# Performance work log

Measured on AMD Instinct MI355X. Metric: run time of the kernel, lower is better.

## Reference

```python
import jax, jax.numpy as jnp
import numpy as np
from jax.scipy.linalg import expm

LATENT, HID, OMEGA, TRANZ, K = 64, 40, 9, 3, 262144


def _linear_params(key, out_d, in_d):
    # equinox Linear default init: U(-1/sqrt(in), 1/sqrt(in)) for weight and bias
    lim = 1.0 / np.sqrt(in_d)
    kw, kb = jax.random.split(key)
    W = jax.random.uniform(kw, (out_d, in_d), minval=-lim, maxval=lim, dtype=jnp.float32)
    b = jax.random.uniform(kb, (out_d,), minval=-lim, maxval=lim, dtype=jnp.float32)
    return W, b


def setup_inputs() -> dict:
    key = jax.random.key(0)
    keys = jax.random.split(key, 7)
    W_o1, b_o1 = _linear_params(keys[0], HID, LATENT)
    W_o2, b_o2 = _linear_params(keys[1], HID, HID)
    W_o3, b_o3 = _linear_params(keys[2], OMEGA, HID)
    W_t1, b_t1 = _linear_params(keys[3], HID, LATENT)
    W_t2, b_t2 = _linear_params(keys[4], HID, HID)
    W_t3, b_t3 = _linear_params(keys[5], TRANZ, HID)
    x = jax.random.normal(keys[6], (LATENT, K), dtype=jnp.float32)
    return {
        "x": x,
        "W_o1": W_o1, "b_o1": b_o1, "W_o2": W_o2, "b_o2": b_o2, "W_o3": W_o3, "b_o3": b_o3,
        "W_t1": W_t1, "b_t1": b_t1, "W_t2": W_t2, "b_t2": b_t2, "W_t3": W_t3, "b_t3": b_t3,
    }


def _exp_omega(omega_flat):
    # omega_flat: (9, K); expm of each column reshaped to 3x3, flattened -> (K, 9)
    f = lambda col: expm(col.reshape(3, 3)).reshape(9)
    return jax.vmap(f, in_axes=1)(omega_flat)


def reference(x, W_o1, b_o1, W_o2, b_o2, W_o3, b_o3,
              W_t1, b_t1, W_t2, b_t2, W_t3, b_t3):
    relu = jax.nn.relu
    # omega branch (note: original applies relu after EVERY layer, incl. last)
    h = relu(W_o1 @ x + b_o1[:, None])
    h = relu(W_o2 @ h + b_o2[:, None])
    omega = relu(W_o3 @ h + b_o3[:, None])          # (9, K)
    rotation = _exp_omega(omega).T                   # (9, K)
    # translation branch
    t = relu(W_t1 @ x + b_t1[:, None])
    t = relu(W_t2 @ t + b_t2[:, None])
    translation = relu(W_t3 @ t + b_t3[:, None])     # (3, K)
    return (omega, rotation, translation)
```

## Files before the change

### kernel.cpp

```cpp
#include <hip/hip_runtime.h>
#include <hip/hip_bf16.h>

#define KC 262144

typedef __attribute__((ext_vector_type(8))) short bf16x8;
typedef __attribute__((ext_vector_type(4))) float f32x4;
typedef unsigned short u16;
typedef unsigned int u32;

__device__ __forceinline__ u16 f2bf(float f) {
    u32 u = __float_as_uint(f);
    return (u16)((u + 0x7fffu + ((u >> 16) & 1u)) >> 16);
}
__device__ __forceinline__ u32 pk2(float a, float b) {
    u16 lo = __bfloat16_as_ushort(__float2bfloat16(a));
    u16 hi = __bfloat16_as_ushort(__float2bfloat16(b));
    return (u32)lo | ((u32)hi << 16);
}
__device__ __forceinline__ float bf2f(u32 h) {
    return __uint_as_float(h << 16);
}

__global__ __launch_bounds__(256) void prep(
    const float* __restrict__ Wo1, const float* __restrict__ bo1,
    const float* __restrict__ Wo2, const float* __restrict__ bo2,
    const float* __restrict__ Wo3, const float* __restrict__ bo3,
    const float* __restrict__ Wt1, const float* __restrict__ bt1,
    const float* __restrict__ Wt2, const float* __restrict__ bt2,
    const float* __restrict__ Wt3, const float* __restrict__ bt3,
    u16* __restrict__ ws)
{
    u16* W1s = ws;
    u16* W2s = ws + 5120;
    u16* W3s = ws + 12800;
    float* b1s = (float*)(ws + 14336);
    const int t0 = blockIdx.x * 256 + threadIdx.x;
    const int NT = gridDim.x * 256;

    for (int i = t0; i < 5120; i += NT) {
        int r = i >> 6, k = i & 63;
        float v = (r < 40) ? Wo1[r * 64 + k] : Wt1[(r - 40) * 64 + k];
        W1s[i] = f2bf(v);
    }
    for (int i = t0; i < 7680; i += NT) {
        int r = i / 96, k = i - r * 96;
        float v = 0.f;
        if (r < 40) {
            if (k < 40) v = Wo2[r * 40 + k];
            else if (k == 80) v = bo2[r];
        } else {
            int rr = r - 40;
            if (k >= 40 && k < 80) v = Wt2[rr * 40 + (k - 40)];
            else if (k == 80) v = bt2[rr];
        }
        W2s[i] = f2bf(v);
    }
    for (int i = t0; i < 1536; i += NT) {
        int r = i / 96, k = i - r * 96;
        float v = 0.f;
        if (r < 9) {
            if (k < 40) v = Wo3[r * 40 + k];
            else if (k == 80) v = bo3[r];
        } else if (r < 12) {
            int rr = r - 9;
            if (k >= 40 && k < 80) v = Wt3[rr * 40 + (k - 40)];
            else if (k == 80) v = bt3[rr];
        }
        W3s[i] = f2bf(v);
    }
    for (int i = t0; i < 80; i += NT)
        b1s[i] = (i < 40) ? bo1[i] : bt1[i - 40];
}

__global__ __launch_bounds__(256, 2) void mlp_mfma(
    const float* __restrict__ x, const u16* __restrict__ ws,
    float* __restrict__ out)
{
    const u16* W1s = ws;
    const u16* W2s = ws + 5120;
    const u16* W3s = ws + 12800;
    const float* b1s = (const float*)(ws + 14336);

    __shared__ float slab[4][64 * 36];

    const int tid = threadIdx.x;
    const int wid = tid >> 6;
    const int lane = tid & 63;
    const int g = lane >> 4;
    const int c = lane & 15;
    const int wgid = blockIdx.x * 4 + wid;
    const int cbase = wgid * 64;

    float* xstage = &slab[wid][0];
    u16* hstp = (u16*)&slab[wid][0];

    bf16x8 A1[5][2], A3[3];
    f32x4 b1v[5];
#pragma unroll
    for (int m = 0; m < 5; ++m) {
#pragma unroll
        for (int s = 0; s < 2; ++s)
            A1[m][s] = *(const bf16x8*)(W1s + (16 * m + c) * 64 + 32 * s + 8 * g);
        b1v[m] = *(const f32x4*)(b1s + 16 * m + 4 * g);
    }
    bf16x8 A2[5][3];
#pragma unroll
    for (int m = 0; m < 5; ++m)
#pragma unroll
        for (int s = 0; s < 3; ++s)
            if (!(s == 0 && m >= 3))
                A2[m][s] = *(const bf16x8*)(W2s + (16 * m + c) * 96 + 32 * s + 8 * g);
#pragma unroll
    for (int s = 0; s < 3; ++s)
        A3[s] = *(const bf16x8*)(W3s + c * 96 + 32 * s + 8 * g);

    const char* gbase = (const char*)x
        + ((size_t)(lane >> 3) * KC + (size_t)(cbase + 4 * (lane & 7))) * 4;
    const int wb = (lane >> 3) * 36 + 4 * (lane & 7);

    u32 w0[4], w1[4];

#pragma unroll
    for (int ch = 0; ch < 2; ++ch) {
        float4 G[8];
#pragma unroll
        for (int i = 0; i < 8; ++i)
            G[i] = *(const float4*)(gbase + (size_t)i * 8 * KC * 4 + ch * 128);
#pragma unroll
        for (int i = 0; i < 8; ++i)
            *(float4*)&xstage[wb + i * 288] = G[i];

        bf16x8 xv[2][2];
#pragma unroll
        for (int tl = 0; tl < 2; ++tl)
#pragma unroll
            for (int s = 0; s < 2; ++s) {
                union { u32 u[4]; bf16x8 v; } uu;
#pragma unroll
                for (int p = 0; p < 4; ++p) {
                    float lo = xstage[(8 * g + 32 * s + 2 * p) * 36 + 16 * tl + c];
                    float hi = xstage[(8 * g + 32 * s + 2 * p + 1) * 36 + 16 * tl + c];
                    uu.u[p] = pk2(lo, hi);
                }
                xv[tl][s] = uu.v;
            }

        {
            uint2 z;
            z.x = (g == 0) ? 0x00003f80u : 0u;
            z.y = 0u;
            *(uint2*)&hstp[c * 120 + 80 + 4 * g] = z;
        }

#pragma unroll
        for (int tl = 0; tl < 2; ++tl) {
            const int gt = 2 * ch + tl;

            f32x4 a1[5];
#pragma unroll
            for (int m = 0; m < 5; ++m) a1[m] = b1v[m];
#pragma unroll
            for (int s = 0; s < 2; ++s)
#pragma unroll
                for (int m = 0; m < 5; ++m)
                    a1[m] = __builtin_amdgcn_mfma_f32_16x16x32_bf16(
                        A1[m][s], xv[tl][s], a1[m], 0, 0, 0);
#pragma unroll
            for (int m = 0; m < 5; ++m) {
                uint2 w;
                w.x = pk2(fmaxf(a1[m][0], 0.f), fmaxf(a1[m][1], 0.f));
                w.y = pk2(fmaxf(a1[m][2], 0.f), fmaxf(a1[m][3], 0.f));
                *(uint2*)&hstp[c * 120 + 16 * m + 4 * g] = w;
            }

            f32x4 a2[5];
#pragma unroll
            for (int m = 0; m < 5; ++m) a2[m] = f32x4{0.f, 0.f, 0.f, 0.f};
#pragma unroll
            for (int s = 0; s < 3; ++s) {
                bf16x8 hb = *(const bf16x8*)&hstp[c * 120 + 32 * s + 8 * g];
#pragma unroll
                for (int m = 0; m < 5; ++m)
                    if (!(s == 0 && m >= 3))
                        a2[m] = __builtin_amdgcn_mfma_f32_16x16x32_bf16(
                            A2[m][s], hb, a2[m], 0, 0, 0);
            }
#pragma unroll
            for (int m = 0; m < 5; ++m) {
                uint2 w;
                w.x = pk2(fmaxf(a2[m][0], 0.f), fmaxf(a2[m][1], 0.f));
                w.y = pk2(fmaxf(a2[m][2], 0.f), fmaxf(a2[m][3], 0.f));
                *(uint2*)&hstp[c * 120 + 16 * m + 4 * g] = w;
            }

            f32x4 a3 = f32x4{0.f, 0.f, 0.f, 0.f};
#pragma unroll
            for (int s = 0; s < 3; ++s) {
                bf16x8 hb = *(const bf16x8*)&hstp[c * 120 + 32 * s + 8 * g];
                a3 = __builtin_amdgcn_mfma_f32_16x16x32_bf16(
                    A3[s], hb, a3, 0, 0, 0);
            }
            w0[gt] = pk2(fmaxf(a3[0], 0.f), fmaxf(a3[1], 0.f));
            w1[gt] = pk2(fmaxf(a3[2], 0.f), fmaxf(a3[3], 0.f));
        }
    }

    {
        const int T = lane >> 4;
        const int cp = lane & 15;
        const int s0 = cp, s1 = 16 + cp, s2 = 32 + cp;

        auto selT = [&](u32 v0, u32 v1, u32 v2, u32 v3) -> u32 {
            u32 lo = (T & 1) ? v1 : v0;
            u32 hi = (T & 1) ? v3 : v2;
            return (T & 2) ? hi : lo;
        };
        u32 q0 = selT((u32)__shfl((int)w0[0], s0), (u32)__shfl((int)w0[1], s0),
                      (u32)__shfl((int)w0[2], s0), (u32)__shfl((int)w0[3], s0));
        u32 q1 = selT((u32)__shfl((int)w1[0], s0), (u32)__shfl((int)w1[1], s0),
                      (u32)__shfl((int)w1[2], s0), (u32)__shfl((int)w1[3], s0));
        u32 q2 = selT((u32)__shfl((int)w0[0], s1), (u32)__shfl((int)w0[1], s1),
                      (u32)__shfl((int)w0[2], s1), (u32)__shfl((int)w0[3], s1));
        u32 q3 = selT((u32)__shfl((int)w1[0], s1), (u32)__shfl((int)w1[1], s1),
                      (u32)__shfl((int)w1[2], s1), (u32)__shfl((int)w1[3], s1));
        u32 q4 = selT((u32)__shfl((int)w0[0], s2), (u32)__shfl((int)w0[1], s2),
                      (u32)__shfl((int)w0[2], s2), (u32)__shfl((int)w0[3], s2));
        u32 q5 = selT((u32)__shfl((int)w1[0], s2), (u32)__shfl((int)w1[1], s2),
                      (u32)__shfl((int)w1[2], s2), (u32)__shfl((int)w1[3], s2));

        float om[9];
        om[0] = bf2f(q0 & 0xffffu); om[1] = bf2f(q0 >> 16);
        om[2] = bf2f(q1 & 0xffffu); om[3] = bf2f(q1 >> 16);
        om[4] = bf2f(q2 & 0xffffu); om[5] = bf2f(q2 >> 16);
        om[6] = bf2f(q3 & 0xffffu); om[7] = bf2f(q3 >> 16);
        om[8] = bf2f(q4 & 0xffffu);
        float tr0 = bf2f(q4 >> 16);
        float tr1 = bf2f(q5 & 0xffffu);
        float tr2 = bf2f(q5 >> 16);

        const size_t ob = (size_t)cbase + lane;
#pragma unroll
        for (int j = 0; j < 9; ++j)
            out[(size_t)j * KC + ob] = om[j];
        out[(size_t)18 * KC + ob] = tr0;
        out[(size_t)19 * KC + ob] = tr1;
        out[(size_t)20 * KC + ob] = tr2;

        float B[9];
#pragma unroll
        for (int i = 0; i < 9; ++i) B[i] = om[i] * (1.0f / 32.0f);
        float T9[9] = {1.f, 0.f, 0.f, 0.f, 1.f, 0.f, 0.f, 0.f, 1.f};
#pragma unroll
        for (int m = 9; m >= 1; --m) {
            float U[9];
#pragma unroll
            for (int rr = 0; rr < 3; ++rr)
#pragma unroll
                for (int cc = 0; cc < 3; ++cc)
                    U[rr * 3 + cc] = B[rr * 3 + 0] * T9[0 * 3 + cc]
                                   + B[rr * 3 + 1] * T9[1 * 3 + cc]
                                   + B[rr * 3 + 2] * T9[2 * 3 + cc];
            const float s = 1.0f / (float)m;
#pragma unroll
            for (int i = 0; i < 9; ++i)
                T9[i] = U[i] * s + ((i == 0 || i == 4 || i == 8) ? 1.0f : 0.0f);
        }
#pragma unroll
        for (int q = 0; q < 5; ++q) {
            float U[9];
#pragma unroll
            for (int rr = 0; rr < 3; ++rr)
#pragma unroll
                for (int cc = 0; cc < 3; ++cc)
                    U[rr * 3 + cc] = T9[rr * 3 + 0] * T9[0 * 3 + cc]
                                   + T9[rr * 3 + 1] * T9[1 * 3 + cc]
                                   + T9[rr * 3 + 2] * T9[2 * 3 + cc];
#pragma unroll
            for (int i = 0; i < 9; ++i) T9[i] = U[i];
        }
#pragma unroll
        for (int j = 0; j < 9; ++j)
            out[(size_t)(9 + j) * KC + ob] = T9[j];
    }
}

extern "C" void kernel_launch(void* const* d_in, const int* in_sizes, int n_in,
                              void* d_out, int out_size, void* d_ws, size_t ws_size,
                              hipStream_t stream) {
    const float* x   = (const float*)d_in[0];
    const float* Wo1 = (const float*)d_in[1];
    const float* bo1 = (const float*)d_in[2];
    const float* Wo2 = (const float*)d_in[3];
    const float* bo2 = (const float*)d_in[4];
    const float* Wo3 = (const float*)d_in[5];
    const float* bo3 = (const float*)d_in[6];
    const float* Wt1 = (const float*)d_in[7];
    const float* bt1 = (const float*)d_in[8];
    const float* Wt2 = (const float*)d_in[9];
    const float* bt2 = (const float*)d_in[10];
    const float* Wt3 = (const float*)d_in[11];
    const float* bt3 = (const float*)d_in[12];

    u16* ws = (u16*)d_ws;
    float* out = (float*)d_out;

    hipLaunchKernelGGL(prep, dim3(16), dim3(256), 0, stream,
                       Wo1, bo1, Wo2, bo2, Wo3, bo3,
                       Wt1, bt1, Wt2, bt2, Wt3, bt3, ws);
    hipLaunchKernelGGL(mlp_mfma, dim3(1024), dim3(256), 0, stream,
                       x, ws, out);
}
```

Baseline: 35.59 us.

## Replace LDS staging with direct register loads and cross-lane shuffle transposes

Removes the per-wave shared memory slab. Each lane now loads its x elements straight from global memory as scalar 4-byte reads in MFMA B-operand order, and the next tile is prefetched in software while the current one computes. Between MLP layers the hidden activations are transposed with __shfl instead of an LDS write/read round trip, and the bias-one row is inserted by select. This drops LDS traffic and its synchronization, but uses narrower global loads, many more shuffle instructions, and more registers.

```diff
diff --git a/kernel.cpp b/kernel.cpp
--- a/kernel.cpp
+++ b/kernel.cpp
@@ -72,7 +72,45 @@
         b1s[i] = (i < 40) ? bo1[i] : bt1[i - 40];
 }
 
-__global__ __launch_bounds__(256, 2) void mlp_mfma(
+__device__ __forceinline__ void transpose_h(
+    const u32* Px, const u32* Py, int g, int c, bf16x8* hb)
+{
+    const int srcA = 16 * (2 * (g & 1)) + c;
+    const int srcB = srcA + 16;
+    const bool hiM = (g >= 2);
+#pragma unroll
+    for (int s = 0; s < 2; ++s) {
+        union { u32 u[4]; bf16x8 v; } uu;
+        u32 a0 = (u32)__shfl((int)Px[2 * s], srcA);
+        u32 b0 = (u32)__shfl((int)Px[2 * s + 1], srcA);
+        uu.u[0] = hiM ? b0 : a0;
+        u32 a1 = (u32)__shfl((int)Py[2 * s], srcA);
+        u32 b1 = (u32)__shfl((int)Py[2 * s + 1], srcA);
+        uu.u[1] = hiM ? b1 : a1;
+        u32 a2 = (u32)__shfl((int)Px[2 * s], srcB);
+        u32 b2 = (u32)__shfl((int)Px[2 * s + 1], srcB);
+        uu.u[2] = hiM ? b2 : a2;
+        u32 a3 = (u32)__shfl((int)Py[2 * s], srcB);
+        u32 b3 = (u32)__shfl((int)Py[2 * s + 1], srcB);
+        uu.u[3] = hiM ? b3 : a3;
+        hb[s] = uu.v;
+    }
+    {
+        union { u32 u[4]; bf16x8 v; } uu;
+        u32 v0 = (u32)__shfl((int)Px[4], srcA);
+        u32 v1 = (u32)__shfl((int)Py[4], srcA);
+        u32 v2 = (u32)__shfl((int)Px[4], srcB);
+        u32 v3 = (u32)__shfl((int)Py[4], srcB);
+        u32 k0 = (g == 2) ? 0x00003f80u : 0u;
+        uu.u[0] = hiM ? k0 : v0;
+        uu.u[1] = hiM ? 0u : v1;
+        uu.u[2] = hiM ? 0u : v2;
+        uu.u[3] = hiM ? 0u : v3;
+        hb[2] = uu.v;
+    }
+}
+
+__global__ __launch_bounds__(256, 2) void mlp_shfl(
     const float* __restrict__ x, const u16* __restrict__ ws,
     float* __restrict__ out)
 {
@@ -81,8 +119,6 @@
     const u16* W3s = ws + 12800;
     const float* b1s = (const float*)(ws + 14336);
 
-    __shared__ float slab[4][64 * 36];
-
     const int tid = threadIdx.x;
     const int wid = tid >> 6;
     const int lane = tid & 63;
@@ -91,9 +127,6 @@
     const int wgid = blockIdx.x * 4 + wid;
     const int cbase = wgid * 64;
 
-    float* xstage = &slab[wid][0];
-    u16* hstp = (u16*)&slab[wid][0];
-
     bf16x8 A1[5][2], A3[3];
     f32x4 b1v[5];
 #pragma unroll
@@ -114,94 +147,89 @@
     for (int s = 0; s < 3; ++s)
         A3[s] = *(const bf16x8*)(W3s + c * 96 + 32 * s + 8 * g);
 
-    const char* gbase = (const char*)x
-        + ((size_t)(lane >> 3) * KC + (size_t)(cbase + 4 * (lane & 7))) * 4;
-    const int wb = (lane >> 3) * 36 + 4 * (lane & 7);
+    u32 xoff[16];
+#pragma unroll
+    for (int jj = 0; jj < 16; ++jj) {
+        int row = 8 * g + (jj & 7) + 32 * (jj >> 3);
+        xoff[jj] = (u32)((row * KC + cbase + c) * 4);
+    }
+    const char* xb_ = (const char*)x;
+
+    float xr[16];
+#pragma unroll
+    for (int jj = 0; jj < 16; ++jj)
+        xr[jj] = *(const float*)(xb_ + xoff[jj]);
 
     u32 w0[4], w1[4];
 
 #pragma unroll
-    for (int ch = 0; ch < 2; ++ch) {
-        float4 G[8];
-#pragma unroll
-        for (int i = 0; i < 8; ++i)
-            G[i] = *(const float4*)(gbase + (size_t)i * 8 * KC * 4 + ch * 128);
-#pragma unroll
-        for (int i = 0; i < 8; ++i)
-            *(float4*)&xstage[wb + i * 288] = G[i];
-
-        bf16x8 xv[2][2];
-#pragma unroll
-        for (int tl = 0; tl < 2; ++tl)
-#pragma unroll
-            for (int s = 0; s < 2; ++s) {
-                union { u32 u[4]; bf16x8 v; } uu;
-#pragma unroll
-                for (int p = 0; p < 4; ++p) {
-                    float lo = xstage[(8 * g + 32 * s + 2 * p) * 36 + 16 * tl + c];
-                    float hi = xstage[(8 * g + 32 * s + 2 * p + 1) * 36 + 16 * tl + c];
-                    uu.u[p] = pk2(lo, hi);
-                }
-                xv[tl][s] = uu.v;
-            }
-
-        {
-            uint2 z;
-            z.x = (g == 0) ? 0x00003f80u : 0u;
-            z.y = 0u;
-            *(uint2*)&hstp[c * 120 + 80 + 4 * g] = z;
-        }
-
-#pragma unroll
-        for (int tl = 0; tl < 2; ++tl) {
-            const int gt = 2 * ch + tl;
-
-            f32x4 a1[5];
-#pragma unroll
-            for (int m = 0; m < 5; ++m) a1[m] = b1v[m];
-#pragma unroll
-            for (int s = 0; s < 2; ++s)
-#pragma unroll
-                for (int m = 0; m < 5; ++m)
-                    a1[m] = __builtin_amdgcn_mfma_f32_16x16x32_bf16(
-                        A1[m][s], xv[tl][s], a1[m], 0, 0, 0);
-#pragma unroll
-            for (int m = 0; m < 5; ++m) {
-                uint2 w;
-                w.x = pk2(fmaxf(a1[m][0], 0.f), fmaxf(a1[m][1], 0.f));
-                w.y = pk2(fmaxf(a1[m][2], 0.f), fmaxf(a1[m][3], 0.f));
-                *(uint2*)&hstp[c * 120 + 16 * m + 4 * g] = w;
-            }
-
-            f32x4 a2[5];
-#pragma unroll
-            for (int m = 0; m < 5; ++m) a2[m] = f32x4{0.f, 0.f, 0.f, 0.f};
-#pragma unroll
-            for (int s = 0; s < 3; ++s) {
-                bf16x8 hb = *(const bf16x8*)&hstp[c * 120 + 32 * s + 8 * g];
-#pragma unroll
-                for (int m = 0; m < 5; ++m)
-                    if (!(s == 0 && m >= 3))
-                        a2[m] = __builtin_amdgcn_mfma_f32_16x16x32_bf16(
-                            A2[m][s], hb, a2[m], 0, 0, 0);
-            }
-#pragma unroll
-            for (int m = 0; m < 5; ++m) {
-                uint2 w;
-                w.x = pk2(fmaxf(a2[m][0], 0.f), fmaxf(a2[m][1], 0.f));
-                w.y = pk2(fmaxf(a2[m][2], 0.f), fmaxf(a2[m][3], 0.f));
-                *(uint2*)&hstp[c * 120 + 16 * m + 4 * g] = w;
-            }
-
-            f32x4 a3 = f32x4{0.f, 0.f, 0.f, 0.f};
-#pragma unroll
-            for (int s = 0; s < 3; ++s) {
-                bf16x8 hb = *(const bf16x8*)&hstp[c * 120 + 32 * s + 8 * g];
-                a3 = __builtin_amdgcn_mfma_f32_16x16x32_bf16(
-                    A3[s], hb, a3, 0, 0, 0);
-            }
-            w0[gt] = pk2(fmaxf(a3[0], 0.f), fmaxf(a3[1], 0.f));
-            w1[gt] = pk2(fmaxf(a3[2], 0.f), fmaxf(a3[3], 0.f));
+    for (int t = 0; t < 4; ++t) {
+        bf16x8 xv[2];
+#pragma unroll
+        for (int s = 0; s < 2; ++s) {
+            union { u32 u[4]; bf16x8 v; } uu;
+#pragma unroll
+            for (int p = 0; p < 4; ++p)
+                uu.u[p] = pk2(xr[8 * s + 2 * p], xr[8 * s + 2 * p + 1]);
+            xv[s] = uu.v;
+        }
+
+        float xrn[16];
+        if (t < 3) {
+#pragma unroll
+            for (int jj = 0; jj < 16; ++jj)
+                xrn[jj] = *(const float*)(xb_ + (xoff[jj] + (t + 1) * 64));
+        }
+
+        f32x4 a1[5];
+#pragma unroll
+        for (int m = 0; m < 5; ++m) a1[m] = b1v[m];
+#pragma unroll
+        for (int s = 0; s < 2; ++s)
+#pragma unroll
+            for (int m = 0; m < 5; ++m)
+                a1[m] = __builtin_amdgcn_mfma_f32_16x16x32_bf16(
+                    A1[m][s], xv[s], a1[m], 0, 0, 0);
+
+        u32 Px[5], Py[5];
+#pragma unroll
+        for (int m = 0; m < 5; ++m) {
+            Px[m] = pk2(fmaxf(a1[m][0], 0.f), fmaxf(a1[m][1], 0.f));
+            Py[m] = pk2(fmaxf(a1[m][2], 0.f), fmaxf(a1[m][3], 0.f));
+        }
+        bf16x8 hb[3];
+        transpose_h(Px, Py, g, c, hb);
+
+        f32x4 a2[5];
+#pragma unroll
+        for (int m = 0; m < 5; ++m) a2[m] = f32x4{0.f, 0.f, 0.f, 0.f};
+#pragma unroll
+        for (int s = 0; s < 3; ++s)
+#pragma unroll
+            for (int m = 0; m < 5; ++m)
+                if (!(s == 0 && m >= 3))
+                    a2[m] = __builtin_amdgcn_mfma_f32_16x16x32_bf16(
+                        A2[m][s], hb[s], a2[m], 0, 0, 0);
+#pragma unroll
+        for (int m = 0; m < 5; ++m) {
+            Px[m] = pk2(fmaxf(a2[m][0], 0.f), fmaxf(a2[m][1], 0.f));
+            Py[m] = pk2(fmaxf(a2[m][2], 0.f), fmaxf(a2[m][3], 0.f));
+        }
+        transpose_h(Px, Py, g, c, hb);
+
+        f32x4 a3 = f32x4{0.f, 0.f, 0.f, 0.f};
+#pragma unroll
+        for (int s = 0; s < 3; ++s)
+            a3 = __builtin_amdgcn_mfma_f32_16x16x32_bf16(
+                A3[s], hb[s], a3, 0, 0, 0);
+
+        w0[t] = pk2(fmaxf(a3[0], 0.f), fmaxf(a3[1], 0.f));
+        w1[t] = pk2(fmaxf(a3[2], 0.f), fmaxf(a3[3], 0.f));
+
+        if (t < 3) {
+#pragma unroll
+            for (int jj = 0; jj < 16; ++jj)
+                xr[jj] = xrn[jj];
         }
     }
 
@@ -307,6 +335,6 @@
     hipLaunchKernelGGL(prep, dim3(16), dim3(256), 0, stream,
                        Wo1, bo1, Wo2, bo2, Wo3, bo3,
                        Wt1, bt1, Wt2, bt2, Wt3, bt3, ws);
-    hipLaunchKernelGGL(mlp_mfma, dim3(1024), dim3(256), 0, stream,
+    hipLaunchKernelGGL(mlp_shfl, dim3(1024), dim3(256), 0, stream,
                        x, ws, out);
 }
```

After: 35.09 us. Within noise of the previous version (-1.4%).
